# Optimization experiments

Hardware: AMD Instinct MI355X
Metric: run time of the kernel (lower is better)

Reference implementation:

```python
import jax, jax.numpy as jnp
import numpy as np

MOMENTUM = 0.5  # update_method='momentum'
EPS = 1e-12


def _l2norm(x):
    return x / jnp.sqrt(jnp.sum(x * x, axis=-1, keepdims=True) + EPS)


def setup_inputs() -> dict:
    key = jax.random.key(0)
    k1, k2, k3, k4, k5 = jax.random.split(key, 5)
    N, D, C, B = 200000, 256, 1000, 256
    inputs = _l2norm(jax.random.normal(k1, (B, D), dtype=jnp.float32))
    features = _l2norm(jax.random.normal(k2, (N, D), dtype=jnp.float32))
    cluster_mean = jax.random.normal(k3, (C, D), dtype=jnp.float32)
    labels = jax.random.randint(k4, (N,), 0, C)
    indexes = jax.random.randint(k5, (B,), 0, N)
    targets = labels[indexes]  # cluster id of each mini-batch sample
    return {
        "inputs": inputs,
        "features": features,
        "cluster_mean": cluster_mean,
        "indexes": indexes,
        "labels": labels,
        "targets": targets,
    }


def reference(inputs, features, cluster_mean, indexes, labels, targets):
    # HM.forward: logits against cluster centroids
    outputs = inputs @ cluster_mean.T  # [B, C]

    # HM.backward side effects (memory-bank maintenance), vectorized:
    # 1) momentum scatter update of the per-instance memory bank + L2 renorm
    new_rows = MOMENTUM * features[indexes] + (1.0 - MOMENTUM) * inputs
    new_rows = _l2norm(new_rows)
    feats = features.at[indexes].set(new_rows)

    # 2) naive cluster-mean recompute (get_mean_conv mean part) for touched clusters
    C = cluster_mean.shape[0]
    sums = jax.ops.segment_sum(feats, labels, num_segments=C)            # [C, D]
    cnts = jax.ops.segment_sum(jnp.ones((feats.shape[0],), feats.dtype), labels, num_segments=C)
    means = sums / jnp.maximum(cnts, 1.0)[:, None]
    touched = jnp.zeros((C,), dtype=bool).at[targets].set(True)
    new_cluster_mean = jnp.where(touched[:, None], means, cluster_mean)

    return outputs, feats, new_cluster_mean
```

## Files before the change

### kernel.cpp

```cpp
#include <hip/hip_runtime.h>

typedef float f32x4 __attribute__((ext_vector_type(4)));

#define B 256
#define D 256
#define N 200000
#define C 1000
#define CM_CHUNKS 8

#define K1_BLOCKS   2048
#define LOGITS_LO   0
#define NEWROWS_LO  256
#define TOUCH_BLK   512
#define HIST_LO     513
#define HIST_BLOCKS 64
#define COPY_LO     577
#define COPY_BLOCKS (K1_BLOCKS - COPY_LO)

#define WS_NEWROWS_OFF  0
#define WS_SUMS_OFF     262144
#define WS_HIST_OFF     1286144
#define WS_TOUCHED_OFF  1290144
#define WS_OFFS_OFF     1294144
#define WS_FILLPOS_OFF  1298144
#define WS_ROWLIST_OFF  1302144
#define ZERO_WORDS      (C * D + C + C)

__global__ __launch_bounds__(256) void k0_zero(int* __restrict__ z) {
    int i = blockIdx.x * 256 + threadIdx.x;
    if (i < ZERO_WORDS) z[i] = 0;
}

__global__ __launch_bounds__(256) void k1_kernel(
    const float* __restrict__ inputs, const float* __restrict__ features,
    const float* __restrict__ cluster_mean, const int* __restrict__ indexes,
    const int* __restrict__ labels, const int* __restrict__ targets,
    float* __restrict__ out_logits, float* __restrict__ out_feats,
    float* __restrict__ new_rows, int* __restrict__ hist, int* __restrict__ touched)
{
    const int blk = blockIdx.x;
    const int t = threadIdx.x;

    __shared__ float sbuf[D];
    __shared__ float wpart[4];
    __shared__ float stot;
    __shared__ int   lh[C];

    if (blk >= COPY_LO) {
        const f32x4* src = (const f32x4*)features;
        f32x4*       dst = (f32x4*)out_feats;
        const int total4 = N * (D / 4);
        const int stride = COPY_BLOCKS * 256;
        int i = (blk - COPY_LO) * 256 + t;
        for (; i + stride < total4; i += 2 * stride) {
            f32x4 v0 = src[i];
            f32x4 v1 = src[i + stride];
            __builtin_nontemporal_store(v0, dst + i);
            __builtin_nontemporal_store(v1, dst + i + stride);
        }
        if (i < total4) __builtin_nontemporal_store(src[i], dst + i);
    } else if (blk < NEWROWS_LO) {
        int b = blk - LOGITS_LO;
        sbuf[t] = inputs[b * D + t];
        __syncthreads();
        const f32x4* cmv = (const f32x4*)cluster_mean;
        for (int c = t; c < C; c += 256) {
            const f32x4* cm = cmv + (size_t)c * 64;
            float a0 = 0.f, a1 = 0.f, a2 = 0.f, a3 = 0.f;
            #pragma unroll 8
            for (int d4 = 0; d4 < 64; ++d4) {
                f32x4 v = cm[d4];
                const float* si = sbuf + d4 * 4;
                a0 += v.x * si[0];
                a1 += v.y * si[1];
                a2 += v.z * si[2];
                a3 += v.w * si[3];
            }
            out_logits[(size_t)b * C + c] = (a0 + a1) + (a2 + a3);
        }
    } else if (blk < TOUCH_BLK) {
        int b = blk - NEWROWS_LO;
        int r = indexes[b];
        float x = 0.5f * features[(size_t)r * D + t] + 0.5f * inputs[b * D + t];
        float s = x * x;
        #pragma unroll
        for (int off = 32; off > 0; off >>= 1) s += __shfl_down(s, off);
        if ((t & 63) == 0) wpart[t >> 6] = s;
        __syncthreads();
        if (t == 0) stot = (wpart[0] + wpart[1]) + (wpart[2] + wpart[3]);
        __syncthreads();
        new_rows[b * D + t] = x / sqrtf(stot + 1e-12f);
    } else if (blk == TOUCH_BLK) {
        if (t < B) touched[targets[t]] = 1;
    } else {
        for (int i = t; i < C; i += 256) lh[i] = 0;
        __syncthreads();
        const int stride = HIST_BLOCKS * 256;
        for (int i = (blk - HIST_LO) * 256 + t; i < N; i += stride)
            atomicAdd(&lh[labels[i]], 1);
        __syncthreads();
        for (int i = t; i < C; i += 256) {
            int v = lh[i];
            if (v) atomicAdd(&hist[i], v);
        }
    }
}

__global__ __launch_bounds__(256) void k2_kernel(
    const int* __restrict__ indexes, const float* __restrict__ new_rows,
    float* __restrict__ out_feats, const int* __restrict__ hist,
    int* __restrict__ offs, int* __restrict__ fillpos)
{
    const int blk = blockIdx.x;
    const int t = threadIdx.x;

    if (blk < 256) {
        __shared__ int sidx[B];
        __shared__ int lose;
        sidx[t] = indexes[t];
        if (t == 0) lose = 0;
        __syncthreads();
        int b = blk;
        int my = sidx[b];
        if (t > b && sidx[t] == my) lose = 1;
        __syncthreads();
        if (!lose) out_feats[(size_t)my * D + t] = new_rows[b * D + t];
    } else {
        __shared__ int swt[4];
        int base = t * 4;
        int h0 = (base + 0 < C) ? hist[base + 0] : 0;
        int h1 = (base + 1 < C) ? hist[base + 1] : 0;
        int h2 = (base + 2 < C) ? hist[base + 2] : 0;
        int h3 = (base + 3 < C) ? hist[base + 3] : 0;
        int tot = h0 + h1 + h2 + h3;
        int lane = t & 63;
        int scan = tot;
        #pragma unroll
        for (int off = 1; off < 64; off <<= 1) {
            int v = __shfl_up(scan, off);
            if (lane >= off) scan += v;
        }
        if (lane == 63) swt[t >> 6] = scan;
        __syncthreads();
        int wbase = 0;
        for (int i = 0; i < (t >> 6); ++i) wbase += swt[i];
        int excl = wbase + scan - tot;
        if (base + 0 < C) { offs[base + 0] = excl;                fillpos[base + 0] = excl; }
        if (base + 1 < C) { offs[base + 1] = excl + h0;           fillpos[base + 1] = excl + h0; }
        if (base + 2 < C) { offs[base + 2] = excl + h0 + h1;      fillpos[base + 2] = excl + h0 + h1; }
        if (base + 3 < C) { offs[base + 3] = excl + h0 + h1 + h2; fillpos[base + 3] = excl + h0 + h1 + h2; }
    }
}

__global__ __launch_bounds__(256) void fill_kernel(
    const int* __restrict__ labels, const int* __restrict__ touched,
    int* __restrict__ fillpos, int* __restrict__ rowlist)
{
    int i = blockIdx.x * 256 + threadIdx.x;
    if (i >= N) return;
    int lab = labels[i];
    if (touched[lab]) {
        int p = atomicAdd(&fillpos[lab], 1);
        rowlist[p] = i;
    }
}

__global__ __launch_bounds__(256) void cm_sum_kernel(
    const float* __restrict__ out_feats, const int* __restrict__ touched,
    const int* __restrict__ hist, const int* __restrict__ offs,
    const int* __restrict__ rowlist, float* __restrict__ sums)
{
    int c = blockIdx.x >> 3;
    int k = blockIdx.x & 7;
    if (!touched[c]) return;
    int cnt = hist[c];
    if (k >= cnt) return;
    int off = offs[c];
    int t = threadIdx.x;
    float acc = 0.0f;
    for (int j = k; j < cnt; j += CM_CHUNKS)
        acc += out_feats[(size_t)rowlist[off + j] * D + t];
    atomicAdd(&sums[(size_t)c * D + t], acc);
}

__global__ __launch_bounds__(256) void means_kernel(
    const float* __restrict__ cluster_mean, const float* __restrict__ sums,
    const int* __restrict__ hist, const int* __restrict__ touched,
    float* __restrict__ out_cm)
{
    int c = blockIdx.x;
    int t = threadIdx.x;
    float out;
    if (touched[c]) out = sums[(size_t)c * D + t] / fmaxf((float)hist[c], 1.0f);
    else            out = cluster_mean[(size_t)c * D + t];
    out_cm[(size_t)c * D + t] = out;
}

extern "C" void kernel_launch(void* const* d_in, const int* in_sizes, int n_in,
                              void* d_out, int out_size, void* d_ws, size_t ws_size,
                              hipStream_t stream) {
    const float* inputs       = (const float*)d_in[0];
    const float* features     = (const float*)d_in[1];
    const float* cluster_mean = (const float*)d_in[2];
    const int*   indexes      = (const int*)d_in[3];
    const int*   labels       = (const int*)d_in[4];
    const int*   targets      = (const int*)d_in[5];

    float* out_logits = (float*)d_out;
    float* out_feats  = out_logits + (size_t)B * C;
    float* out_cm     = out_feats + (size_t)N * D;

    char* ws = (char*)d_ws;
    float* new_rows = (float*)(ws + WS_NEWROWS_OFF);
    float* sums     = (float*)(ws + WS_SUMS_OFF);
    int*   hist     = (int*)(ws + WS_HIST_OFF);
    int*   touched  = (int*)(ws + WS_TOUCHED_OFF);
    int*   offs     = (int*)(ws + WS_OFFS_OFF);
    int*   fillpos  = (int*)(ws + WS_FILLPOS_OFF);
    int*   rowlist  = (int*)(ws + WS_ROWLIST_OFF);

    k0_zero<<<(ZERO_WORDS + 255) / 256, 256, 0, stream>>>((int*)(ws + WS_SUMS_OFF));
    k1_kernel<<<K1_BLOCKS, 256, 0, stream>>>(inputs, features, cluster_mean,
                                             indexes, labels, targets,
                                             out_logits, out_feats, new_rows,
                                             hist, touched);
    k2_kernel<<<257, 256, 0, stream>>>(indexes, new_rows, out_feats,
                                       hist, offs, fillpos);
    fill_kernel<<<(N + 255) / 256, 256, 0, stream>>>(labels, touched, fillpos, rowlist);
    cm_sum_kernel<<<C * CM_CHUNKS, 256, 0, stream>>>(out_feats, touched, hist,
                                                     offs, rowlist, sums);
    means_kernel<<<C, 256, 0, stream>>>(cluster_mean, sums, hist, touched, out_cm);
}
```

Measured before the change: 133.7 us.

## Fuse cluster sum and mean kernels into one block-reduced kernel, unroll copy loop

Replaces the atomic-based cluster sum kernel plus separate means kernel with a single 1024-thread-per-cluster kernel that reduces partial sums in shared memory and writes the mean directly. This removes the sums workspace, its zeroing, the global atomics and one kernel launch. The feature copy loop is also unrolled from 2 to 4 loads in flight, and shared-memory declarations are scoped per branch. The costs are fewer blocks per cluster (1000 blocks of 1024 threads instead of 8000 blocks of 256) and a block-wide barrier.

```diff
diff --git a/kernel.cpp b/kernel.cpp
--- a/kernel.cpp
+++ b/kernel.cpp
@@ -6,7 +6,6 @@
 #define D 256
 #define N 200000
 #define C 1000
-#define CM_CHUNKS 8
 
 #define K1_BLOCKS   2048
 #define LOGITS_LO   0
@@ -18,13 +17,12 @@
 #define COPY_BLOCKS (K1_BLOCKS - COPY_LO)
 
 #define WS_NEWROWS_OFF  0
-#define WS_SUMS_OFF     262144
-#define WS_HIST_OFF     1286144
-#define WS_TOUCHED_OFF  1290144
-#define WS_OFFS_OFF     1294144
-#define WS_FILLPOS_OFF  1298144
-#define WS_ROWLIST_OFF  1302144
-#define ZERO_WORDS      (C * D + C + C)
+#define WS_HIST_OFF     262144
+#define WS_TOUCHED_OFF  266144
+#define WS_OFFS_OFF     270144
+#define WS_FILLPOS_OFF  274144
+#define WS_ROWLIST_OFF  278144
+#define ZERO_WORDS      (2 * C)
 
 __global__ __launch_bounds__(256) void k0_zero(int* __restrict__ z) {
     int i = blockIdx.x * 256 + threadIdx.x;
@@ -41,25 +39,26 @@
     const int blk = blockIdx.x;
     const int t = threadIdx.x;
 
-    __shared__ float sbuf[D];
-    __shared__ float wpart[4];
-    __shared__ float stot;
-    __shared__ int   lh[C];
-
     if (blk >= COPY_LO) {
         const f32x4* src = (const f32x4*)features;
         f32x4*       dst = (f32x4*)out_feats;
         const int total4 = N * (D / 4);
         const int stride = COPY_BLOCKS * 256;
         int i = (blk - COPY_LO) * 256 + t;
-        for (; i + stride < total4; i += 2 * stride) {
+        for (; i + 3 * stride < total4; i += 4 * stride) {
             f32x4 v0 = src[i];
             f32x4 v1 = src[i + stride];
+            f32x4 v2 = src[i + 2 * stride];
+            f32x4 v3 = src[i + 3 * stride];
             __builtin_nontemporal_store(v0, dst + i);
             __builtin_nontemporal_store(v1, dst + i + stride);
-        }
-        if (i < total4) __builtin_nontemporal_store(src[i], dst + i);
+            __builtin_nontemporal_store(v2, dst + i + 2 * stride);
+            __builtin_nontemporal_store(v3, dst + i + 3 * stride);
+        }
+        for (; i < total4; i += stride)
+            __builtin_nontemporal_store(src[i], dst + i);
     } else if (blk < NEWROWS_LO) {
+        __shared__ float sbuf[D];
         int b = blk - LOGITS_LO;
         sbuf[t] = inputs[b * D + t];
         __syncthreads();
@@ -79,6 +78,8 @@
             out_logits[(size_t)b * C + c] = (a0 + a1) + (a2 + a3);
         }
     } else if (blk < TOUCH_BLK) {
+        __shared__ float wpart[4];
+        __shared__ float stot;
         int b = blk - NEWROWS_LO;
         int r = indexes[b];
         float x = 0.5f * features[(size_t)r * D + t] + 0.5f * inputs[b * D + t];
@@ -93,6 +94,7 @@
     } else if (blk == TOUCH_BLK) {
         if (t < B) touched[targets[t]] = 1;
     } else {
+        __shared__ int lh[C];
         for (int i = t; i < C; i += 256) lh[i] = 0;
         __syncthreads();
         const int stride = HIST_BLOCKS * 256;
@@ -165,35 +167,32 @@
     }
 }
 
-__global__ __launch_bounds__(256) void cm_sum_kernel(
-    const float* __restrict__ out_feats, const int* __restrict__ touched,
-    const int* __restrict__ hist, const int* __restrict__ offs,
-    const int* __restrict__ rowlist, float* __restrict__ sums)
-{
-    int c = blockIdx.x >> 3;
-    int k = blockIdx.x & 7;
-    if (!touched[c]) return;
-    int cnt = hist[c];
-    if (k >= cnt) return;
-    int off = offs[c];
-    int t = threadIdx.x;
+__global__ __launch_bounds__(1024) void cm_kernel(
+    const float* __restrict__ cluster_mean, const float* __restrict__ out_feats,
+    const int* __restrict__ touched, const int* __restrict__ hist,
+    const int* __restrict__ offs, const int* __restrict__ rowlist,
+    float* __restrict__ out_cm)
+{
+    const int c = blockIdx.x;
+    const int d = threadIdx.x & 255;
+    const int k = threadIdx.x >> 8;
+    if (!touched[c]) {
+        if (k == 0) out_cm[(size_t)c * D + d] = cluster_mean[(size_t)c * D + d];
+        return;
+    }
+    __shared__ float red[3][256];
+    const int cnt = hist[c];
+    const int off = offs[c];
     float acc = 0.0f;
-    for (int j = k; j < cnt; j += CM_CHUNKS)
-        acc += out_feats[(size_t)rowlist[off + j] * D + t];
-    atomicAdd(&sums[(size_t)c * D + t], acc);
-}
-
-__global__ __launch_bounds__(256) void means_kernel(
-    const float* __restrict__ cluster_mean, const float* __restrict__ sums,
-    const int* __restrict__ hist, const int* __restrict__ touched,
-    float* __restrict__ out_cm)
-{
-    int c = blockIdx.x;
-    int t = threadIdx.x;
-    float out;
-    if (touched[c]) out = sums[(size_t)c * D + t] / fmaxf((float)hist[c], 1.0f);
-    else            out = cluster_mean[(size_t)c * D + t];
-    out_cm[(size_t)c * D + t] = out;
+    #pragma unroll 4
+    for (int j = k; j < cnt; j += 4)
+        acc += out_feats[(size_t)rowlist[off + j] * D + d];
+    if (k > 0) red[k - 1][d] = acc;
+    __syncthreads();
+    if (k == 0) {
+        float tot = acc + red[0][d] + red[1][d] + red[2][d];
+        out_cm[(size_t)c * D + d] = tot / fmaxf((float)cnt, 1.0f);
+    }
 }
 
 extern "C" void kernel_launch(void* const* d_in, const int* in_sizes, int n_in,
@@ -212,14 +211,13 @@
 
     char* ws = (char*)d_ws;
     float* new_rows = (float*)(ws + WS_NEWROWS_OFF);
-    float* sums     = (float*)(ws + WS_SUMS_OFF);
     int*   hist     = (int*)(ws + WS_HIST_OFF);
     int*   touched  = (int*)(ws + WS_TOUCHED_OFF);
     int*   offs     = (int*)(ws + WS_OFFS_OFF);
     int*   fillpos  = (int*)(ws + WS_FILLPOS_OFF);
     int*   rowlist  = (int*)(ws + WS_ROWLIST_OFF);
 
-    k0_zero<<<(ZERO_WORDS + 255) / 256, 256, 0, stream>>>((int*)(ws + WS_SUMS_OFF));
+    k0_zero<<<(ZERO_WORDS + 255) / 256, 256, 0, stream>>>((int*)(ws + WS_HIST_OFF));
     k1_kernel<<<K1_BLOCKS, 256, 0, stream>>>(inputs, features, cluster_mean,
                                              indexes, labels, targets,
                                              out_logits, out_feats, new_rows,
@@ -227,7 +225,6 @@
     k2_kernel<<<257, 256, 0, stream>>>(indexes, new_rows, out_feats,
                                        hist, offs, fillpos);
     fill_kernel<<<(N + 255) / 256, 256, 0, stream>>>(labels, touched, fillpos, rowlist);
-    cm_sum_kernel<<<C * CM_CHUNKS, 256, 0, stream>>>(out_feats, touched, hist,
-                                                     offs, rowlist, sums);
-    means_kernel<<<C, 256, 0, stream>>>(cluster_mean, sums, hist, touched, out_cm);
-}
+    cm_kernel<<<C, 1024, 0, stream>>>(cluster_mean, out_feats, touched, hist,
+                                      offs, rowlist, out_cm);
+}
```

Result: faster. 125.3 us (-6.3%).
